# Optimization experiments

Hardware: AMD Instinct MI355X
Metric: run time of the kernel (lower is better)

Reference implementation:

```python
import jax, jax.numpy as jnp
import numpy as np

NHEADS = 16  # init kwarg


def setup_inputs() -> dict:
    key = jax.random.key(0)
    ks = jax.random.split(key, 3)
    S, B, E = 2048, 4, 1024
    x = jax.random.normal(ks[0], (S, B, E), dtype=jnp.float32)
    Wqkv = jax.random.normal(ks[1], (E, 3 * E), dtype=jnp.float32) * 0.02
    bqkv = jnp.zeros((3 * E,), dtype=jnp.float32)
    Wout = jax.random.normal(ks[2], (E, E), dtype=jnp.float32) * 0.02
    bout = jnp.zeros((E,), dtype=jnp.float32)
    return {"x": x, "Wqkv": Wqkv, "bqkv": bqkv, "Wout": Wout, "bout": bout}


def reference(x, Wqkv, bqkv, Wout, bout):
    S, B, E = x.shape
    H = NHEADS
    d = E // H
    scale = jnp.sqrt(jnp.asarray(E / H, dtype=x.dtype))  # sqrt(d_head)
    qkv = x @ Wqkv + bqkv                      # (S, B, 3E)
    q, k, v = jnp.split(qkv, 3, axis=-1)       # each (S, B, E)
    # (S, B, E) -> (S, B*H, d) -> (B*H, S, d), matching torch reshape+permute
    q = q.reshape(S, B * H, d).transpose(1, 0, 2)
    k = k.reshape(S, B * H, d).transpose(1, 0, 2)
    v = v.reshape(S, B * H, d).transpose(1, 0, 2)
    scores = jnp.einsum('hsd,htd->hst', q, k) / scale  # (B*H, S, S)
    attn = jax.nn.softmax(scores, axis=-1)
    o = jnp.einsum('hst,htd->hsd', attn, v)    # (B*H, S, d)
    o = o.transpose(1, 0, 2).reshape(S, B, E)  # back to (S, B, E)
    return o @ Wout + bout
```

## Files before the change

kernel.cpp:

```cpp
#include <hip/hip_runtime.h>

typedef short s16x8 __attribute__((ext_vector_type(8)));
typedef float f32x4 __attribute__((ext_vector_type(4)));
typedef float f32x16 __attribute__((ext_vector_type(16)));
typedef unsigned int u32x2 __attribute__((ext_vector_type(2)));
typedef unsigned int u32x4 __attribute__((ext_vector_type(4)));

__device__ inline float bf2f(unsigned short u) {
    union { float f; unsigned int i; } x; x.i = ((unsigned int)u) << 16; return x.f;
}
__device__ inline unsigned short f2bf(float f) {
    union { float f; unsigned int i; } x; x.f = f;
    unsigned int r = x.i + 0x7fff + ((x.i >> 16) & 1);
    return (unsigned short)(r >> 16);
}
__device__ inline unsigned int pack_bf16(float a, float b) {
    unsigned int ia = __float_as_uint(a) + 0x8000u;
    unsigned int ib = __float_as_uint(b) + 0x8000u;
    return __builtin_amdgcn_perm(ib, ia, 0x07060302u);
}

__device__ inline void gload_lds16(const unsigned short* g, unsigned short* l) {
    __builtin_amdgcn_global_load_lds(
        (const __attribute__((address_space(1))) unsigned int*)g,
        (__attribute__((address_space(3))) unsigned int*)l, 16, 0, 0);
}

__global__ __launch_bounds__(256) void prep_kernel(
    const void* __restrict__ x, const void* __restrict__ Wqkv,
    const void* __restrict__ bqkv, const void* __restrict__ Wout,
    const void* __restrict__ bout,
    unsigned short* __restrict__ xb, unsigned short* __restrict__ WqkvT,
    unsigned short* __restrict__ WoutT, float* __restrict__ bq_f,
    float* __restrict__ bo_f, int* __restrict__ flag) {
    __shared__ int s[256];
    __shared__ unsigned short t[64][72];
    int tid = threadIdx.x;
    int bid = blockIdx.x;

    const unsigned short* x16 = (const unsigned short*)x;
    int cnt = 0;
#pragma unroll
    for (int k = 0; k < 4; ++k) {
        unsigned short u = x16[2 * (tid * 4 + k)];
        int e = (u >> 7) & 0xFF;
        if (e >= 117 && e <= 129) cnt++;
    }
    s[tid] = cnt;
    __syncthreads();
    for (int off = 128; off; off >>= 1) {
        if (tid < off) s[tid] += s[tid + off];
        __syncthreads();
    }
    int mode = (s[0] < 512) ? 1 : 0;

    if (bid < 4096) {
        int i0 = bid * 2048 + tid * 8;
        if (mode) {
            const f32x4* f = (const f32x4*)x;
            f32x4 a = f[i0 >> 2];
            f32x4 c = f[(i0 >> 2) + 1];
            u32x4 o;
            o[0] = pack_bf16(a[0], a[1]);
            o[1] = pack_bf16(a[2], a[3]);
            o[2] = pack_bf16(c[0], c[1]);
            o[3] = pack_bf16(c[2], c[3]);
            *(u32x4*)(xb + i0) = o;
        } else {
            *(s16x8*)(xb + i0) = *(const s16x8*)((const unsigned short*)x + i0);
        }
        return;
    }
    if (bid < 5120) {
        const void* in;
        unsigned short* out;
        int R = 1024, C, bx, by;
        if (bid < 4864) {
            in = Wqkv; out = WqkvT; C = 3072;
            int b2 = bid - 4096; bx = b2 % 48; by = b2 / 48;
        } else {
            in = Wout; out = WoutT; C = 1024;
            int b2 = bid - 4864; bx = b2 % 16; by = b2 / 16;
        }
        int r0 = by * 64, c0 = bx * 64;
        for (int i = tid; i < 512; i += 256) {
            int r = i >> 3, c8 = (i & 7) * 8;
            size_t idx = (size_t)(r0 + r) * C + (c0 + c8);
            if (mode) {
                const float* fin = (const float*)in + idx;
                f32x4 a = *(const f32x4*)fin;
                f32x4 c = *(const f32x4*)(fin + 4);
                u32x4 o;
                o[0] = pack_bf16(a[0], a[1]);
                o[1] = pack_bf16(a[2], a[3]);
                o[2] = pack_bf16(c[0], c[1]);
                o[3] = pack_bf16(c[2], c[3]);
                *(u32x4*)&t[r][c8] = o;
            } else {
                *(s16x8*)&t[r][c8] = *(const s16x8*)((const unsigned short*)in + idx);
            }
        }
        __syncthreads();
        for (int i = tid; i < 512; i += 256) {
            int c = i >> 3, r8 = (i & 7) * 8;
            s16x8 v;
#pragma unroll
            for (int j = 0; j < 8; ++j) v[j] = t[r8 + j][c];
            *(s16x8*)(out + (size_t)(c0 + c) * R + r0 + r8) = v;
        }
        return;
    }
    if (bid < 5136) {
        int i = (bid - 5120) * 256 + tid;
        if (i < 3072)
            bq_f[i] = mode ? ((const float*)bqkv)[i] : bf2f(((const unsigned short*)bqkv)[i]);
        else {
            int j = i - 3072;
            bo_f[j] = mode ? ((const float*)bout)[j] : bf2f(((const unsigned short*)bout)[j]);
        }
        return;
    }
    if (tid == 0) *flag = mode;
}

__global__ __launch_bounds__(256) void transpose_v(
    const unsigned short* __restrict__ qkv, unsigned short* __restrict__ Vt) {
    __shared__ unsigned short t[64][72];
    int bh = blockIdx.y; int b = bh >> 4, h = bh & 15;
    int k0 = blockIdx.x * 64;
    int tid = threadIdx.x;
    int kr = tid >> 2, db = (tid & 3) * 16;
    const unsigned short* src = qkv + ((size_t)(k0 + kr) * 4 + b) * 3072 + 2048 + h * 64 + db;
    *(s16x8*)&t[kr][db] = *(const s16x8*)src;
    *(s16x8*)&t[kr][db + 8] = *(const s16x8*)(src + 8);
    __syncthreads();
    int d = tid >> 2, kb = (tid & 3) * 16;
    unsigned short* dst = Vt + (size_t)bh * 131072 + (size_t)d * 2048 + k0 + kb;
    s16x8 a, c;
#pragma unroll
    for (int j = 0; j < 8; ++j) a[j] = t[kb + j][d];
#pragma unroll
    for (int j = 0; j < 8; ++j) c[j] = t[kb + 8 + j][d];
    *(s16x8*)dst = a;
    *(s16x8*)(dst + 8) = c;
}

__global__ __launch_bounds__(512) void gemm_pipe_kernel(
    const unsigned short* __restrict__ A, const unsigned short* __restrict__ BT,
    const float* __restrict__ bias, void* __restrict__ Cout,
    int M, int N, int K, int qcols, float qscale, const int* __restrict__ outf32flag) {
    __shared__ unsigned short As[3][256 * 64];
    __shared__ unsigned short Bs[3][128 * 64];
    int tid = threadIdx.x;
    int lane = tid & 63, w = tid >> 6;
    int wr = w >> 1, wc = w & 1;
    int g = lane >> 4, qh = lane & 15;
    int m0 = blockIdx.y * 256, n0 = blockIdx.x * 128;
    int vxor = (lane & 7) ^ (lane >> 3);
    int axor = qh & 7;

    f32x4 z = {0.f, 0.f, 0.f, 0.f};
    f32x4 acc[4][4];
#pragma unroll
    for (int m = 0; m < 4; ++m)
#pragma unroll
        for (int n = 0; n < 4; ++n) acc[m][n] = z;

    const unsigned short* Asrc = A + (size_t)(m0 + w * 8 + (lane >> 3)) * K + vxor * 8;
    const unsigned short* Bsrc = BT + (size_t)(n0 + w * 8 + (lane >> 3)) * K + vxor * 8;

#define STAGE_A(buf, t, j) gload_lds16(Asrc + (size_t)(j) * 64 * K + (size_t)(t) * 64, \
                                       &As[buf][0] + (j) * 4096 + w * 512)
#define STAGE_B(buf, t, j) gload_lds16(Bsrc + (size_t)(j) * 64 * K + (size_t)(t) * 64, \
                                       &Bs[buf][0] + (j) * 4096 + w * 512)

    int NT = K >> 6;
    STAGE_A(0, 0, 0); STAGE_A(0, 0, 1); STAGE_A(0, 0, 2); STAGE_A(0, 0, 3);
    STAGE_B(0, 0, 0); STAGE_B(0, 0, 1);
    STAGE_A(1, 1, 0); STAGE_A(1, 1, 1); STAGE_A(1, 1, 2); STAGE_A(1, 1, 3);
    STAGE_B(1, 1, 0); STAGE_B(1, 1, 1);
    asm volatile("s_waitcnt vmcnt(6)" ::: "memory");
    __builtin_amdgcn_s_barrier();

    int cur = 0;
    for (int t = 0; t < NT; ++t) {
        int nx = cur + 2; if (nx >= 3) nx -= 3;
        bool pf = (t + 2) < NT;
        const unsigned short* Ab = &As[cur][0];
        const unsigned short* Bb = &Bs[cur][0];

        s16x8 bf[4][2];
#pragma unroll
        for (int n = 0; n < 4; ++n)
#pragma unroll
            for (int kk = 0; kk < 2; ++kk)
                bf[n][kk] = *(const s16x8*)(Bb + (size_t)(wc * 64 + n * 16 + qh) * 64 +
                                            (((kk * 4 + g) ^ axor) * 8));

        if (pf) { STAGE_A(nx, t + 2, 0); STAGE_A(nx, t + 2, 1); STAGE_B(nx, t + 2, 0); }
        {
            s16x8 af[2][2];
#pragma unroll
            for (int i = 0; i < 2; ++i)
#pragma unroll
                for (int kk = 0; kk < 2; ++kk)
                    af[i][kk] = *(const s16x8*)(Ab + (size_t)(wr * 64 + i * 16 + qh) * 64 +
                                                (((kk * 4 + g) ^ axor) * 8));
            __builtin_amdgcn_s_setprio(1);
#pragma unroll
            for (int kk = 0; kk < 2; ++kk)
#pragma unroll
                for (int i = 0; i < 2; ++i)
#pragma unroll
                    for (int n = 0; n < 4; ++n)
                        acc[i][n] = __builtin_amdgcn_mfma_f32_16x16x32_bf16(af[i][kk], bf[n][kk], acc[i][n], 0, 0, 0);
            __builtin_amdgcn_s_setprio(0);
        }

        if (pf) { STAGE_A(nx, t + 2, 2); STAGE_A(nx, t + 2, 3); STAGE_B(nx, t + 2, 1); }
        {
            s16x8 af[2][2];
#pragma unroll
            for (int i = 0; i < 2; ++i)
#pragma unroll
                for (int kk = 0; kk < 2; ++kk)
                    af[i][kk] = *(const s16x8*)(Ab + (size_t)(wr * 64 + (i + 2) * 16 + qh) * 64 +
                                                (((kk * 4 + g) ^ axor) * 8));
            __builtin_amdgcn_s_setprio(1);
#pragma unroll
            for (int kk = 0; kk < 2; ++kk)
#pragma unroll
                for (int i = 0; i < 2; ++i)
#pragma unroll
                    for (int n = 0; n < 4; ++n)
                        acc[i + 2][n] = __builtin_amdgcn_mfma_f32_16x16x32_bf16(af[i][kk], bf[n][kk], acc[i + 2][n], 0, 0, 0);
            __builtin_amdgcn_s_setprio(0);
        }
        if (t + 1 < NT) {
            if (pf) asm volatile("s_waitcnt vmcnt(6)" ::: "memory");
            else    asm volatile("s_waitcnt vmcnt(0)" ::: "memory");
            __builtin_amdgcn_s_barrier();
        }
        cur = cur + 1; if (cur >= 3) cur -= 3;
    }
#undef STAGE_A
#undef STAGE_B

    bool f32out = (outf32flag != nullptr) && (*outf32flag != 0);
    int crow0 = m0 + wr * 64;
    int ccol0 = n0 + wc * 64;
#pragma unroll
    for (int n = 0; n < 4; ++n) {
        int col = ccol0 + n * 16 + qh;
        float bv = bias[col];
        float qs = (col < qcols) ? qscale : 1.0f;
#pragma unroll
        for (int m = 0; m < 4; ++m) {
            int rbase = crow0 + m * 16 + g * 4;
#pragma unroll
            for (int qq = 0; qq < 4; ++qq) {
                float v = (acc[m][n][qq] + bv) * qs;
                if (f32out)
                    ((float*)Cout)[(size_t)(rbase + qq) * N + col] = v;
                else
                    ((unsigned short*)Cout)[(size_t)(rbase + qq) * N + col] = f2bf(v);
            }
        }
    }
}

__global__ __launch_bounds__(256) void attn_kernel(
    const unsigned short* __restrict__ qkv, const unsigned short* __restrict__ Vt,
    unsigned short* __restrict__ O) {
    int L = blockIdx.y * 16 + blockIdx.x;
    int xcd = L & 7;
    int i = L >> 3;
    int bh = xcd * 8 + (i & 7);
    int q0 = (i >> 3) << 7;
    int b = bh >> 4, h = bh & 15;
    int tid = threadIdx.x, lane = tid & 63, w = tid >> 6;
    int l31 = lane & 31, l5 = lane >> 5;

    __shared__ unsigned short Ks[8 * 128 * 8];
    __shared__ unsigned short Vs[64 * 16 * 8];

    int qrow = q0 + w * 32 + l31;
    const unsigned short* qp = qkv + ((size_t)qrow * 4 + b) * 3072 + h * 64 + l5 * 8;
    s16x8 qf[4];
#pragma unroll
    for (int st = 0; st < 4; ++st) qf[st] = *(const s16x8*)(qp + st * 16);

    f32x16 z16 = {0.f,0.f,0.f,0.f,0.f,0.f,0.f,0.f,0.f,0.f,0.f,0.f,0.f,0.f,0.f,0.f};
    f32x16 oacc[2];
    oacc[0] = z16; oacc[1] = z16;
    float lrun = 0.f;

    const unsigned short* kbase = qkv + ((size_t)lane * 4 + b) * 3072 + 1024 + h * 64;
    const unsigned short* vbase[4];
#pragma unroll
    for (int j = 0; j < 4; ++j) {
        int id = j * 256 + w * 64 + (tid & 63);
        int d = id >> 4, blk = id & 15;
        vbase[j] = Vt + (size_t)bh * 131072 + (size_t)d * 2048 + ((blk ^ (d & 7)) * 8);
    }

    for (int t = 0; t < 16; ++t) {
        __syncthreads();
#pragma unroll
        for (int j = 0; j < 4; ++j) {
            int gd = w * 2 + (j & 1);
            int khalf = j >> 1;
            gload_lds16(kbase + (size_t)khalf * 786432 + gd * 8,
                        Ks + ((size_t)gd * 128 + khalf * 64) * 8);
        }
#pragma unroll
        for (int j = 0; j < 4; ++j) {
            gload_lds16(vbase[j], Vs + (size_t)(j * 256 + w * 64) * 8);
            vbase[j] += 128;
        }
        kbase += 1572864;
        __syncthreads();

#pragma unroll
        for (int kt = 0; kt < 4; ++kt) {
            f32x16 sc = z16;
#pragma unroll
            for (int st = 0; st < 4; ++st) {
                int gd = st * 2 + l5;
                s16x8 kf = *(const s16x8*)(Ks + ((size_t)gd * 128 + kt * 32 + l31) * 8);
                sc = __builtin_amdgcn_mfma_f32_32x32x16_bf16(kf, qf[st], sc, 0, 0, 0);
            }
            float p[16];
#pragma unroll
            for (int r = 0; r < 16; ++r) {
                p[r] = __builtin_amdgcn_exp2f(sc[r]);
                lrun += p[r];
            }
#pragma unroll
            for (int ks1 = 0; ks1 < 2; ++ks1) {
                unsigned int A0 = pack_bf16(p[8 * ks1 + 0], p[8 * ks1 + 1]);
                unsigned int A1 = pack_bf16(p[8 * ks1 + 2], p[8 * ks1 + 3]);
                unsigned int B0 = pack_bf16(p[8 * ks1 + 4], p[8 * ks1 + 5]);
                unsigned int B1 = pack_bf16(p[8 * ks1 + 6], p[8 * ks1 + 7]);
                u32x2 r0 = __builtin_amdgcn_permlane32_swap(A0, B0, false, false);
                u32x2 r1 = __builtin_amdgcn_permlane32_swap(A1, B1, false, false);
                union { unsigned int u[4]; s16x8 v; } uu;
                uu.u[0] = r0[0];
                uu.u[1] = r1[0];
                uu.u[2] = r0[1];
                uu.u[3] = r1[1];
                int ks = kt * 2 + ks1;
#pragma unroll
                for (int dt = 0; dt < 2; ++dt) {
                    int d = dt * 32 + l31;
                    int kb = (ks * 2 + l5) ^ (d & 7);
                    s16x8 vf = *(const s16x8*)(Vs + ((size_t)d * 16 + kb) * 8);
                    oacc[dt] = __builtin_amdgcn_mfma_f32_32x32x16_bf16(vf, uu.v, oacc[dt], 0, 0, 0);
                }
            }
        }
    }

    lrun += __shfl_xor(lrun, 32);

    float rl = 1.f / lrun;
    unsigned short* orow = O + ((size_t)qrow * 4 + b) * 1024 + h * 64 + l5 * 4;
#pragma unroll
    for (int dt = 0; dt < 2; ++dt) {
#pragma unroll
        for (int g2 = 0; g2 < 4; ++g2) {
            u32x2 pv;
            pv[0] = pack_bf16(oacc[dt][4 * g2 + 0] * rl, oacc[dt][4 * g2 + 1] * rl);
            pv[1] = pack_bf16(oacc[dt][4 * g2 + 2] * rl, oacc[dt][4 * g2 + 3] * rl);
            *(u32x2*)(orow + dt * 32 + g2 * 8) = pv;
        }
    }
}

extern "C" void kernel_launch(void* const* d_in, const int* in_sizes, int n_in,
                              void* d_out, int out_size, void* d_ws, size_t ws_size,
                              hipStream_t stream) {
    const void* x    = d_in[0];
    const void* Wqkv = d_in[1];
    const void* bqkv = d_in[2];
    const void* Wout = d_in[3];
    const void* bout = d_in[4];

    char* ws = (char*)d_ws;
    unsigned short* qkv   = (unsigned short*)(ws);
    unsigned short* Obuf  = (unsigned short*)(ws + 50331648);
    unsigned short* WqkvT = (unsigned short*)(ws + 67108864);
    unsigned short* WoutT = (unsigned short*)(ws + 73400320);
    unsigned short* xb    = (unsigned short*)(ws + 75497472);
    unsigned short* Vtg   = xb;
    float*          bq_f  = (float*)(ws + 92274688);
    float*          bo_f  = (float*)(ws + 92286976);
    int*            flag  = (int*)(ws + 92291072);

    prep_kernel<<<5137, 256, 0, stream>>>(x, Wqkv, bqkv, Wout, bout,
                                          xb, WqkvT, WoutT, bq_f, bo_f, flag);

    gemm_pipe_kernel<<<dim3(24, 32), 512, 0, stream>>>(xb, WqkvT, bq_f, qkv,
                                                       8192, 3072, 1024, 1024, 0.18033688f, nullptr);
    transpose_v<<<dim3(32, 64), 256, 0, stream>>>(qkv, Vtg);
    attn_kernel<<<dim3(16, 64), 256, 0, stream>>>(qkv, Vtg, Obuf);
    gemm_pipe_kernel<<<dim3(8, 32), 512, 0, stream>>>(Obuf, WoutT, bo_f, d_out,
                                                      8192, 1024, 1024, 0, 1.0f, flag);
}
```

Baseline: 244.4 us.

## Load attention K/V fragments directly from global with per-head K relayout

Extends the V-transpose kernel so it also copies K into a contiguous per-(batch, head) layout. The attention kernel then drops its LDS staging buffers and both per-tile barriers, and each wave reads its K and V MFMA fragments straight from global memory in a 64-step loop. The aim is to remove LDS round-trips and block-level synchronisation. In exchange, all four waves of a block now fetch the same K/V data through the cache separately, global-load latency sits directly in the MFMA chain with only an unroll of 2 to hide it, and the relayout kernel writes an extra K copy.

```diff
diff --git a/kernel.cpp b/kernel.cpp
--- a/kernel.cpp
+++ b/kernel.cpp
@@ -123,12 +123,22 @@
     if (tid == 0) *flag = mode;
 }
 
-__global__ __launch_bounds__(256) void transpose_v(
-    const unsigned short* __restrict__ qkv, unsigned short* __restrict__ Vt) {
+__global__ __launch_bounds__(256) void relayout_kv(
+    const unsigned short* __restrict__ qkv, unsigned short* __restrict__ Kl,
+    unsigned short* __restrict__ Vt) {
     __shared__ unsigned short t[64][72];
     int bh = blockIdx.y; int b = bh >> 4, h = bh & 15;
     int k0 = blockIdx.x * 64;
     int tid = threadIdx.x;
+
+    {
+        int kk2 = tid >> 2, cc = (tid & 3) * 16;
+        const unsigned short* ksrc = qkv + ((size_t)(k0 + kk2) * 4 + b) * 3072 + 1024 + h * 64 + cc;
+        unsigned short* kdst = Kl + (size_t)bh * 131072 + (size_t)(k0 + kk2) * 64 + cc;
+        *(s16x8*)kdst = *(const s16x8*)ksrc;
+        *(s16x8*)(kdst + 8) = *(const s16x8*)(ksrc + 8);
+    }
+
     int kr = tid >> 2, db = (tid & 3) * 16;
     const unsigned short* src = qkv + ((size_t)(k0 + kr) * 4 + b) * 3072 + 2048 + h * 64 + db;
     *(s16x8*)&t[kr][db] = *(const s16x8*)src;
@@ -270,8 +280,8 @@
 }
 
 __global__ __launch_bounds__(256) void attn_kernel(
-    const unsigned short* __restrict__ qkv, const unsigned short* __restrict__ Vt,
-    unsigned short* __restrict__ O) {
+    const unsigned short* __restrict__ qkv, const unsigned short* __restrict__ Kl,
+    const unsigned short* __restrict__ Vt, unsigned short* __restrict__ O) {
     int L = blockIdx.y * 16 + blockIdx.x;
     int xcd = L & 7;
     int i = L >> 3;
@@ -281,9 +291,6 @@
     int tid = threadIdx.x, lane = tid & 63, w = tid >> 6;
     int l31 = lane & 31, l5 = lane >> 5;
 
-    __shared__ unsigned short Ks[8 * 128 * 8];
-    __shared__ unsigned short Vs[64 * 16 * 8];
-
     int qrow = q0 + w * 32 + l31;
     const unsigned short* qp = qkv + ((size_t)qrow * 4 + b) * 3072 + h * 64 + l5 * 8;
     s16x8 qf[4];
@@ -295,68 +302,40 @@
     oacc[0] = z16; oacc[1] = z16;
     float lrun = 0.f;
 
-    const unsigned short* kbase = qkv + ((size_t)lane * 4 + b) * 3072 + 1024 + h * 64;
-    const unsigned short* vbase[4];
-#pragma unroll
-    for (int j = 0; j < 4; ++j) {
-        int id = j * 256 + w * 64 + (tid & 63);
-        int d = id >> 4, blk = id & 15;
-        vbase[j] = Vt + (size_t)bh * 131072 + (size_t)d * 2048 + ((blk ^ (d & 7)) * 8);
-    }
-
-    for (int t = 0; t < 16; ++t) {
-        __syncthreads();
-#pragma unroll
-        for (int j = 0; j < 4; ++j) {
-            int gd = w * 2 + (j & 1);
-            int khalf = j >> 1;
-            gload_lds16(kbase + (size_t)khalf * 786432 + gd * 8,
-                        Ks + ((size_t)gd * 128 + khalf * 64) * 8);
-        }
-#pragma unroll
-        for (int j = 0; j < 4; ++j) {
-            gload_lds16(vbase[j], Vs + (size_t)(j * 256 + w * 64) * 8);
-            vbase[j] += 128;
-        }
-        kbase += 1572864;
-        __syncthreads();
-
-#pragma unroll
-        for (int kt = 0; kt < 4; ++kt) {
-            f32x16 sc = z16;
-#pragma unroll
-            for (int st = 0; st < 4; ++st) {
-                int gd = st * 2 + l5;
-                s16x8 kf = *(const s16x8*)(Ks + ((size_t)gd * 128 + kt * 32 + l31) * 8);
-                sc = __builtin_amdgcn_mfma_f32_32x32x16_bf16(kf, qf[st], sc, 0, 0, 0);
-            }
-            float p[16];
-#pragma unroll
-            for (int r = 0; r < 16; ++r) {
-                p[r] = __builtin_amdgcn_exp2f(sc[r]);
-                lrun += p[r];
-            }
-#pragma unroll
-            for (int ks1 = 0; ks1 < 2; ++ks1) {
-                unsigned int A0 = pack_bf16(p[8 * ks1 + 0], p[8 * ks1 + 1]);
-                unsigned int A1 = pack_bf16(p[8 * ks1 + 2], p[8 * ks1 + 3]);
-                unsigned int B0 = pack_bf16(p[8 * ks1 + 4], p[8 * ks1 + 5]);
-                unsigned int B1 = pack_bf16(p[8 * ks1 + 6], p[8 * ks1 + 7]);
-                u32x2 r0 = __builtin_amdgcn_permlane32_swap(A0, B0, false, false);
-                u32x2 r1 = __builtin_amdgcn_permlane32_swap(A1, B1, false, false);
-                union { unsigned int u[4]; s16x8 v; } uu;
-                uu.u[0] = r0[0];
-                uu.u[1] = r1[0];
-                uu.u[2] = r0[1];
-                uu.u[3] = r1[1];
-                int ks = kt * 2 + ks1;
-#pragma unroll
-                for (int dt = 0; dt < 2; ++dt) {
-                    int d = dt * 32 + l31;
-                    int kb = (ks * 2 + l5) ^ (d & 7);
-                    s16x8 vf = *(const s16x8*)(Vs + ((size_t)d * 16 + kb) * 8);
-                    oacc[dt] = __builtin_amdgcn_mfma_f32_32x32x16_bf16(vf, uu.v, oacc[dt], 0, 0, 0);
-                }
+    const unsigned short* Kb = Kl + (size_t)bh * 131072 + (size_t)l31 * 64 + l5 * 8;
+    const unsigned short* Vb = Vt + (size_t)bh * 131072 + (size_t)l31 * 2048 + l5 * 8;
+
+#pragma unroll 2
+    for (int sl = 0; sl < 64; ++sl) {
+        f32x16 sc = z16;
+#pragma unroll
+        for (int st = 0; st < 4; ++st) {
+            s16x8 kf = *(const s16x8*)(Kb + (size_t)sl * 2048 + st * 16);
+            sc = __builtin_amdgcn_mfma_f32_32x32x16_bf16(kf, qf[st], sc, 0, 0, 0);
+        }
+        float p[16];
+#pragma unroll
+        for (int r = 0; r < 16; ++r) {
+            p[r] = __builtin_amdgcn_exp2f(sc[r]);
+            lrun += p[r];
+        }
+#pragma unroll
+        for (int ks1 = 0; ks1 < 2; ++ks1) {
+            unsigned int A0 = pack_bf16(p[8 * ks1 + 0], p[8 * ks1 + 1]);
+            unsigned int A1 = pack_bf16(p[8 * ks1 + 2], p[8 * ks1 + 3]);
+            unsigned int B0 = pack_bf16(p[8 * ks1 + 4], p[8 * ks1 + 5]);
+            unsigned int B1 = pack_bf16(p[8 * ks1 + 6], p[8 * ks1 + 7]);
+            u32x2 r0 = __builtin_amdgcn_permlane32_swap(A0, B0, false, false);
+            u32x2 r1 = __builtin_amdgcn_permlane32_swap(A1, B1, false, false);
+            union { unsigned int u[4]; s16x8 v; } uu;
+            uu.u[0] = r0[0];
+            uu.u[1] = r1[0];
+            uu.u[2] = r0[1];
+            uu.u[3] = r1[1];
+#pragma unroll
+            for (int dt = 0; dt < 2; ++dt) {
+                s16x8 vf = *(const s16x8*)(Vb + (size_t)dt * 65536 + sl * 32 + ks1 * 16);
+                oacc[dt] = __builtin_amdgcn_mfma_f32_32x32x16_bf16(vf, uu.v, oacc[dt], 0, 0, 0);
             }
         }
     }
@@ -396,14 +375,15 @@
     float*          bq_f  = (float*)(ws + 92274688);
     float*          bo_f  = (float*)(ws + 92286976);
     int*            flag  = (int*)(ws + 92291072);
+    unsigned short* Klg   = (unsigned short*)(ws + 92295168);
 
     prep_kernel<<<5137, 256, 0, stream>>>(x, Wqkv, bqkv, Wout, bout,
                                           xb, WqkvT, WoutT, bq_f, bo_f, flag);
 
     gemm_pipe_kernel<<<dim3(24, 32), 512, 0, stream>>>(xb, WqkvT, bq_f, qkv,
                                                        8192, 3072, 1024, 1024, 0.18033688f, nullptr);
-    transpose_v<<<dim3(32, 64), 256, 0, stream>>>(qkv, Vtg);
-    attn_kernel<<<dim3(16, 64), 256, 0, stream>>>(qkv, Vtg, Obuf);
+    relayout_kv<<<dim3(32, 64), 256, 0, stream>>>(qkv, Klg, Vtg);
+    attn_kernel<<<dim3(16, 64), 256, 0, stream>>>(qkv, Klg, Vtg, Obuf);
     gemm_pipe_kernel<<<dim3(8, 32), 512, 0, stream>>>(Obuf, WoutT, bo_f, d_out,
                                                       8192, 1024, 1024, 0, 1.0f, flag);
 }
```

New measurement: 432.1 us. 1.77x slower.
